# Kernel optimization log

Measured on AMD Instinct MI355X. Metric: run time of the kernel, lower is better.

## Reference

```python
import jax, jax.numpy as jnp
import numpy as np

B, H, N, Dh = 4, 16, 8192, 64
EPS = 1e-5          # masked-fill epsilon for D
CLAMP_EPS = 1e-10   # clamp_abs epsilon for gamma denominator
PROJ_EPS = 4e-3     # geoopt float32 projection epsilon


def _sumsq(x):
    return jnp.sum(x * x, axis=-1, keepdims=True)


def _pt0back(x, v, k):
    # geoopt parallel_transport0back: transport v from x back to origin
    # = v * lambda_x / lambda_0 = v / (1 + k ||x||^2)
    return v / jnp.maximum(1.0 + k * _sumsq(x), 1e-15)


def _lambda_x(x, k):
    # conformal factor 2 / (1 + k ||x||^2)
    return 2.0 / jnp.maximum(1.0 + k * _sumsq(x), 1e-15)


def _clamp_abs(x, eps):
    s = jnp.where(x >= 0, 1.0, -1.0)
    return s * jnp.maximum(jnp.abs(x), eps)


def _project(x, k):
    # clip points to the ball of radius (1-eps)/sqrt(|k|) when k < 0
    maxnorm = jnp.where(k < 0, (1.0 - PROJ_EPS) / jnp.sqrt(jnp.abs(k) + 1e-15), 1e15)
    norm = jnp.maximum(jnp.linalg.norm(x, axis=-1, keepdims=True), 1e-15)
    return jnp.where(norm > maxnorm, x / norm * maxnorm, x)


def _artan_k(u, k):
    sk = jnp.sqrt(jnp.abs(k) + 1e-15)
    su = sk * u
    hyp = jnp.arctanh(jnp.clip(su, -1.0 + 1e-7, 1.0 - 1e-7))
    return jnp.where(k < 0, hyp, jnp.arctan(su)) / sk


def _tan_k(u, k):
    sk = jnp.sqrt(jnp.abs(k) + 1e-15)
    su = sk * u
    return jnp.where(k < 0, jnp.tanh(su), jnp.tan(su)) / sk


def _mobius_scalar_mul(r, x, k):
    xnorm = jnp.maximum(jnp.linalg.norm(x, axis=-1, keepdims=True), 1e-15)
    return _tan_k(r * _artan_k(xnorm, k), k) * x / xnorm


def setup_inputs() -> dict:
    key = jax.random.key(0)
    kq, kk, kv = jax.random.split(key, 3)
    Q = 0.5 * jax.random.normal(kq, (B, H, N, Dh), dtype=jnp.float32)
    K = 0.5 * jax.random.normal(kk, (B, H, N, Dh), dtype=jnp.float32)
    # scale V so points lie well inside the Poincare ball: ||V||^2 ~ 0.16 < 1/|k|
    V = 0.05 * jax.random.normal(kv, (B, H, N, Dh), dtype=jnp.float32)
    mask = jnp.ones((N,), dtype=jnp.float32)
    curvatures = jnp.linspace(-2.0, -0.5, H, dtype=jnp.float32).reshape(H, 1, 1)
    return {"Q": Q, "K": K, "V": V, "mask": mask, "curvatures": curvatures}


def reference(Q, K, V, mask, curvatures):
    k = curvatures                      # [H,1,1], broadcasts over [B,H,N,1]
    m = mask[None, :, None]             # [1,N,1] -> broadcasts over [B,H,N,D]
    v1 = _pt0back(V, Q, k)              # transport Q from V back to origin
    v2 = _pt0back(V, K, k)
    gamma = _lambda_x(V, k)             # [B,H,N,1]
    denom = _clamp_abs(gamma - 1.0, CLAMP_EPS)
    x = gamma / denom * V * m           # [B,H,N,D]
    v1 = jax.nn.elu(v1) + 1.0           # positive feature map
    v2 = denom * (jax.nn.elu(v2) + 1.0) * m
    v2_sum = jnp.sum(v2, axis=-2)       # [B,H,D]
    Dn = jnp.einsum('bhnd,bhd->bhn', v1, v2_sum)
    D_inv = 1.0 / jnp.where(Dn == 0, EPS, Dn)
    context = jnp.einsum('bhnd,bhne->bhde', v2, x)          # [B,H,D,D]
    X = jnp.einsum('bhde,bhnd,bhn->bhne', context, v1, D_inv)
    X = _project(X, k)
    X = _mobius_scalar_mul(0.5, X, k)
    X = _project(X, k)
    return X
```

## Files before the change

kernel.cpp:

```cpp
#include <hip/hip_runtime.h>
#include <math.h>

#define NROWS   8192
#define DHH     64
#define BHCOUNT 64
#define HCOUNT  16
#define SPLITA  16
#define CHUNKA  (NROWS / SPLITA)
#define GA      32
#define LSTR    68
#define SPLITB  32
#define CHUNKB  (NROWS / SPLITB)
#define CTXSZ   4160
#define EPS_DN  1e-5f
#define PROJ_EPS 0.004f

__device__ __forceinline__ float elu1(float x) {
    return x > 0.0f ? x + 1.0f : expf(x);
}

__global__ __launch_bounds__(256) void phaseA(
        const float* __restrict__ Kp, const float* __restrict__ Vp,
        const float* __restrict__ maskp, const float* __restrict__ curvp,
        float* __restrict__ denomWs, float* __restrict__ partials) {
    __shared__ __align__(16) float v2s[GA * LSTR];
    __shared__ __align__(16) float xs[GA * LSTR];
    const int bx = blockIdx.x;
    const int bh = bx / SPLITA, sp = bx % SPLITA;
    const float k = curvp[bh % HCOUNT];
    const int t = threadIdx.x;
    const int rowBase = sp * CHUNKA;
    const float* Kb = Kp + (size_t)bh * NROWS * DHH;
    const float* Vb = Vp + (size_t)bh * NROWS * DHH;

    float acc[4][4] = {{0.f,0.f,0.f,0.f},{0.f,0.f,0.f,0.f},{0.f,0.f,0.f,0.f},{0.f,0.f,0.f,0.f}};
    float4 v2sum4 = make_float4(0.f, 0.f, 0.f, 0.f);
    const int rloc = t >> 4;
    const int c4   = t & 15;
    const int td   = t >> 4;
    const int te   = t & 15;

    for (int g = 0; g < CHUNKA / GA; ++g) {
        #pragma unroll
        for (int pass = 0; pass < 2; ++pass) {
            const int rl = pass * 16 + rloc;
            const int n = rowBase + g * GA + rl;
            const float4 v4 = *(const float4*)(Vb + (size_t)n * DHH + 4 * c4);
            const float4 k4 = *(const float4*)(Kb + (size_t)n * DHH + 4 * c4);
            float ss = v4.x*v4.x + v4.y*v4.y + v4.z*v4.z + v4.w*v4.w;
            ss += __shfl_xor(ss, 1);
            ss += __shfl_xor(ss, 2);
            ss += __shfl_xor(ss, 4);
            ss += __shfl_xor(ss, 8);
            const float dv    = fmaxf(1.0f + k * ss, 1e-15f);
            const float gamma = 2.0f / dv;
            const float gm1   = gamma - 1.0f;
            const float dnm   = (gm1 >= 0.0f ? 1.0f : -1.0f) * fmaxf(fabsf(gm1), 1e-10f);
            const float m     = maskp[n];
            const float idv   = 1.0f / dv;
            const float cv2   = dnm * m;
            const float cx    = (gamma / dnm) * m;
            float4 v2v, xv;
            v2v.x = cv2 * elu1(k4.x * idv);
            v2v.y = cv2 * elu1(k4.y * idv);
            v2v.z = cv2 * elu1(k4.z * idv);
            v2v.w = cv2 * elu1(k4.w * idv);
            xv.x = cx * v4.x; xv.y = cx * v4.y; xv.z = cx * v4.z; xv.w = cx * v4.w;
            *(float4*)&v2s[rl * LSTR + 4 * c4] = v2v;
            *(float4*)&xs [rl * LSTR + 4 * c4] = xv;
            v2sum4.x += v2v.x; v2sum4.y += v2v.y; v2sum4.z += v2v.z; v2sum4.w += v2v.w;
            if (c4 == 0) denomWs[(size_t)bh * NROWS + n] = dv;
        }
        __syncthreads();
        #pragma unroll 4
        for (int r = 0; r < GA; ++r) {
            const float4 a = *(const float4*)&v2s[r * LSTR + 4 * td];
            const float4 b = *(const float4*)&xs [r * LSTR + 4 * te];
            acc[0][0] += a.x*b.x; acc[0][1] += a.x*b.y; acc[0][2] += a.x*b.z; acc[0][3] += a.x*b.w;
            acc[1][0] += a.y*b.x; acc[1][1] += a.y*b.y; acc[1][2] += a.y*b.z; acc[1][3] += a.y*b.w;
            acc[2][0] += a.z*b.x; acc[2][1] += a.z*b.y; acc[2][2] += a.z*b.z; acc[2][3] += a.z*b.w;
            acc[3][0] += a.w*b.x; acc[3][1] += a.w*b.y; acc[3][2] += a.w*b.z; acc[3][3] += a.w*b.w;
        }
        __syncthreads();
    }

    float* pbase = partials + (size_t)(bh * SPLITA + sp) * CTXSZ;
    #pragma unroll
    for (int i = 0; i < 4; ++i) {
        float4 o = make_float4(acc[i][0], acc[i][1], acc[i][2], acc[i][3]);
        *(float4*)(pbase + (4 * td + i) * DHH + 4 * te) = o;
    }
    __syncthreads();
    *(float4*)&v2s[t * 4] = v2sum4;
    __syncthreads();
    if (t < DHH) {
        const int cc = t >> 2, j = t & 3;
        float s = 0.f;
        #pragma unroll
        for (int q = 0; q < 16; ++q) s += v2s[(q * 16 + cc) * 4 + j];
        pbase[4096 + t] = s;
    }
}

__global__ __launch_bounds__(256) void reduceCtx(
        const float* __restrict__ partials, float* __restrict__ ctxsum) {
    const int bh = blockIdx.x;
    const int t = threadIdx.x;
    for (int idx = t; idx < CTXSZ; idx += 256) {
        const float* p = partials + (size_t)bh * SPLITA * CTXSZ + idx;
        float s = 0.f;
        #pragma unroll
        for (int sp = 0; sp < SPLITA; ++sp) s += p[(size_t)sp * CTXSZ];
        ctxsum[(size_t)bh * CTXSZ + idx] = s;
    }
}

__global__ __launch_bounds__(256) void phaseB(
        const float* __restrict__ Qp, const float* __restrict__ curvp,
        const float* __restrict__ denomWs, const float* __restrict__ ctxsum,
        float* __restrict__ outp) {
    __shared__ __align__(16) float ctx[DHH * LSTR];
    __shared__ __align__(16) float v1s[64 * LSTR];
    __shared__ __align__(16) float v2sum[DHH];
    __shared__ float dinv[64];
    __shared__ float rowsq[64 * 17];
    __shared__ float factor[64];

    const int bx = blockIdx.x;
    const int bh = bx / SPLITB, sp = bx % SPLITB;
    const float k = curvp[bh % HCOUNT];
    const float sk = sqrtf(fabsf(k) + 1e-15f);
    const float maxnorm = (k < 0.0f) ? (1.0f - PROJ_EPS) / sk : 1e15f;
    const int t = threadIdx.x;

    const float* cb = ctxsum + (size_t)bh * CTXSZ;
    #pragma unroll
    for (int i = 0; i < 16; ++i) {
        const int idx = i * 256 + t;
        ctx[(idx >> 6) * LSTR + (idx & 63)] = cb[idx];
    }
    if (t < DHH) v2sum[t] = cb[4096 + t];
    __syncthreads();

    const float* Qb  = Qp  + (size_t)bh * NROWS * DHH;
    float*       Ob  = outp + (size_t)bh * NROWS * DHH;
    const float* dvb = denomWs + (size_t)bh * NROWS;
    const int rloc = t >> 4, c4 = t & 15;
    const int tr = t >> 4, tc = t & 15;

    for (int tile = 0; tile < CHUNKB / 64; ++tile) {
        const int n0 = sp * CHUNKB + tile * 64;
        #pragma unroll
        for (int pass = 0; pass < 4; ++pass) {
            const int rl = pass * 16 + rloc;
            const int n = n0 + rl;
            const float4 q4 = *(const float4*)(Qb + (size_t)n * DHH + 4 * c4);
            const float dv = dvb[n];
            const float idv = 1.0f / dv;
            float4 v14;
            v14.x = elu1(q4.x * idv);
            v14.y = elu1(q4.y * idv);
            v14.z = elu1(q4.z * idv);
            v14.w = elu1(q4.w * idv);
            *(float4*)&v1s[rl * LSTR + 4 * c4] = v14;
            const float4 vs = *(const float4*)&v2sum[4 * c4];
            float dn = v14.x * vs.x + v14.y * vs.y + v14.z * vs.z + v14.w * vs.w;
            dn += __shfl_xor(dn, 1);
            dn += __shfl_xor(dn, 2);
            dn += __shfl_xor(dn, 4);
            dn += __shfl_xor(dn, 8);
            if (c4 == 0) {
                const float Dd = (dn == 0.0f) ? EPS_DN : dn;
                dinv[rl] = 1.0f / Dd;
            }
        }
        __syncthreads();
        float acc[4][4] = {{0.f,0.f,0.f,0.f},{0.f,0.f,0.f,0.f},{0.f,0.f,0.f,0.f},{0.f,0.f,0.f,0.f}};
        #pragma unroll 8
        for (int d = 0; d < DHH; ++d) {
            const float4 cv = *(const float4*)&ctx[d * LSTR + 4 * tc];
            const float a0 = v1s[(4 * tr + 0) * LSTR + d];
            const float a1 = v1s[(4 * tr + 1) * LSTR + d];
            const float a2 = v1s[(4 * tr + 2) * LSTR + d];
            const float a3 = v1s[(4 * tr + 3) * LSTR + d];
            acc[0][0] += a0*cv.x; acc[0][1] += a0*cv.y; acc[0][2] += a0*cv.z; acc[0][3] += a0*cv.w;
            acc[1][0] += a1*cv.x; acc[1][1] += a1*cv.y; acc[1][2] += a1*cv.z; acc[1][3] += a1*cv.w;
            acc[2][0] += a2*cv.x; acc[2][1] += a2*cv.y; acc[2][2] += a2*cv.z; acc[2][3] += a2*cv.w;
            acc[3][0] += a3*cv.x; acc[3][1] += a3*cv.y; acc[3][2] += a3*cv.z; acc[3][3] += a3*cv.w;
        }
        #pragma unroll
        for (int i = 0; i < 4; ++i) {
            const float di = dinv[4 * tr + i];
            acc[i][0] *= di; acc[i][1] *= di; acc[i][2] *= di; acc[i][3] *= di;
            const float ps = acc[i][0]*acc[i][0] + acc[i][1]*acc[i][1]
                           + acc[i][2]*acc[i][2] + acc[i][3]*acc[i][3];
            rowsq[(4 * tr + i) * 17 + tc] = ps;
        }
        __syncthreads();
        if (t < 64) {
            float s = 0.f;
            #pragma unroll
            for (int q = 0; q < 16; ++q) s += rowsq[t * 17 + q];
            const float norm = fmaxf(sqrtf(s), 1e-15f);
            const float f1 = (norm > maxnorm) ? (maxnorm / norm) : 1.0f;
            const float n2 = norm * f1;
            const float xnorm = fmaxf(n2, 1e-15f);
            const float su = sk * xnorm;
            const float suc = fminf(su, 1.0f - 1e-7f);
            float tk;
            if (k < 0.0f) tk = tanhf(0.5f * atanhf(suc));
            else          tk = tanf(0.5f * atanf(su));
            tk = tk / sk;
            const float f2 = tk / xnorm;
            const float n3 = fmaxf(fabsf(tk), 1e-15f);
            const float f3 = (n3 > maxnorm) ? (maxnorm / n3) : 1.0f;
            factor[t] = f1 * f2 * f3;
        }
        __syncthreads();
        #pragma unroll
        for (int i = 0; i < 4; ++i) {
            const float f = factor[4 * tr + i];
            float4 o = make_float4(acc[i][0] * f, acc[i][1] * f, acc[i][2] * f, acc[i][3] * f);
            *(float4*)(Ob + (size_t)(n0 + 4 * tr + i) * DHH + 4 * tc) = o;
        }
        __syncthreads();
    }
}

extern "C" void kernel_launch(void* const* d_in, const int* in_sizes, int n_in,
                              void* d_out, int out_size, void* d_ws, size_t ws_size,
                              hipStream_t stream) {
    const float* Q    = (const float*)d_in[0];
    const float* K    = (const float*)d_in[1];
    const float* V    = (const float*)d_in[2];
    const float* mask = (const float*)d_in[3];
    const float* curv = (const float*)d_in[4];
    float* out = (float*)d_out;

    float* denomWs  = (float*)d_ws;
    float* partials = denomWs + (size_t)BHCOUNT * NROWS;
    float* ctxsum   = partials + (size_t)BHCOUNT * SPLITA * CTXSZ;

    phaseA<<<dim3(BHCOUNT * SPLITA), dim3(256), 0, stream>>>(K, V, mask, curv, denomWs, partials);
    reduceCtx<<<dim3(BHCOUNT), dim3(256), 0, stream>>>(partials, ctxsum);
    phaseB<<<dim3(BHCOUNT * SPLITB), dim3(256), 0, stream>>>(Q, curv, denomWs, ctxsum, out);
}
```

Baseline: 471.7 us.

## Replace partials reduction with atomics and streamline phaseB epilogue

PhaseA now accumulates context and v2 sums into a zeroed buffer with float atomicAdd instead of writing per-split partials, and a separate reduceCtx kernel. SPLITA doubles for more blocks. PhaseB keeps D_inv in registers, reduces row norms with warp shuffles instead of shared memory plus two barriers, uses float4 reads of v1 in the matmul, and replaces tanh(0.5*atanh) with an algebraic half-angle formula. Atomics make summation order nondeterministic and add contention, and a zero-fill kernel is added.

Result: slower. 534.2 us (+13.2%).

```diff
diff --git a/kernel.cpp b/kernel.cpp
--- a/kernel.cpp
+++ b/kernel.cpp
@@ -5,7 +5,7 @@
 #define DHH     64
 #define BHCOUNT 64
 #define HCOUNT  16
-#define SPLITA  16
+#define SPLITA  32
 #define CHUNKA  (NROWS / SPLITA)
 #define GA      32
 #define LSTR    68
@@ -19,10 +19,15 @@
     return x > 0.0f ? x + 1.0f : expf(x);
 }
 
+__global__ __launch_bounds__(256) void zeroCtx(float* __restrict__ p, int n) {
+    const int i = blockIdx.x * 256 + threadIdx.x;
+    if (i < n) p[i] = 0.0f;
+}
+
 __global__ __launch_bounds__(256) void phaseA(
         const float* __restrict__ Kp, const float* __restrict__ Vp,
         const float* __restrict__ maskp, const float* __restrict__ curvp,
-        float* __restrict__ denomWs, float* __restrict__ partials) {
+        float* __restrict__ denomWs, float* __restrict__ ctxsum) {
     __shared__ __align__(16) float v2s[GA * LSTR];
     __shared__ __align__(16) float xs[GA * LSTR];
     const int bx = blockIdx.x;
@@ -84,11 +89,13 @@
         __syncthreads();
     }
 
-    float* pbase = partials + (size_t)(bh * SPLITA + sp) * CTXSZ;
+    float* cbase = ctxsum + (size_t)bh * CTXSZ;
     #pragma unroll
     for (int i = 0; i < 4; ++i) {
-        float4 o = make_float4(acc[i][0], acc[i][1], acc[i][2], acc[i][3]);
-        *(float4*)(pbase + (4 * td + i) * DHH + 4 * te) = o;
+        atomicAdd(&cbase[(4 * td + i) * DHH + 4 * te + 0], acc[i][0]);
+        atomicAdd(&cbase[(4 * td + i) * DHH + 4 * te + 1], acc[i][1]);
+        atomicAdd(&cbase[(4 * td + i) * DHH + 4 * te + 2], acc[i][2]);
+        atomicAdd(&cbase[(4 * td + i) * DHH + 4 * te + 3], acc[i][3]);
     }
     __syncthreads();
     *(float4*)&v2s[t * 4] = v2sum4;
@@ -98,20 +105,7 @@
         float s = 0.f;
         #pragma unroll
         for (int q = 0; q < 16; ++q) s += v2s[(q * 16 + cc) * 4 + j];
-        pbase[4096 + t] = s;
-    }
-}
-
-__global__ __launch_bounds__(256) void reduceCtx(
-        const float* __restrict__ partials, float* __restrict__ ctxsum) {
-    const int bh = blockIdx.x;
-    const int t = threadIdx.x;
-    for (int idx = t; idx < CTXSZ; idx += 256) {
-        const float* p = partials + (size_t)bh * SPLITA * CTXSZ + idx;
-        float s = 0.f;
-        #pragma unroll
-        for (int sp = 0; sp < SPLITA; ++sp) s += p[(size_t)sp * CTXSZ];
-        ctxsum[(size_t)bh * CTXSZ + idx] = s;
+        atomicAdd(&cbase[4096 + t], s);
     }
 }
 
@@ -122,9 +116,6 @@
     __shared__ __align__(16) float ctx[DHH * LSTR];
     __shared__ __align__(16) float v1s[64 * LSTR];
     __shared__ __align__(16) float v2sum[DHH];
-    __shared__ float dinv[64];
-    __shared__ float rowsq[64 * 17];
-    __shared__ float factor[64];
 
     const int bx = blockIdx.x;
     const int bh = bx / SPLITB, sp = bx % SPLITB;
@@ -132,6 +123,7 @@
     const float sk = sqrtf(fabsf(k) + 1e-15f);
     const float maxnorm = (k < 0.0f) ? (1.0f - PROJ_EPS) / sk : 1e15f;
     const int t = threadIdx.x;
+    const int tr = t >> 4, tc = t & 15;
 
     const float* cb = ctxsum + (size_t)bh * CTXSZ;
     #pragma unroll
@@ -145,82 +137,73 @@
     const float* Qb  = Qp  + (size_t)bh * NROWS * DHH;
     float*       Ob  = outp + (size_t)bh * NROWS * DHH;
     const float* dvb = denomWs + (size_t)bh * NROWS;
-    const int rloc = t >> 4, c4 = t & 15;
-    const int tr = t >> 4, tc = t & 15;
 
     for (int tile = 0; tile < CHUNKB / 64; ++tile) {
         const int n0 = sp * CHUNKB + tile * 64;
+        float di[4];
         #pragma unroll
         for (int pass = 0; pass < 4; ++pass) {
-            const int rl = pass * 16 + rloc;
+            const int rl = 4 * tr + pass;
             const int n = n0 + rl;
-            const float4 q4 = *(const float4*)(Qb + (size_t)n * DHH + 4 * c4);
-            const float dv = dvb[n];
-            const float idv = 1.0f / dv;
+            const float4 q4 = *(const float4*)(Qb + (size_t)n * DHH + 4 * tc);
+            const float idv = 1.0f / dvb[n];
             float4 v14;
             v14.x = elu1(q4.x * idv);
             v14.y = elu1(q4.y * idv);
             v14.z = elu1(q4.z * idv);
             v14.w = elu1(q4.w * idv);
-            *(float4*)&v1s[rl * LSTR + 4 * c4] = v14;
-            const float4 vs = *(const float4*)&v2sum[4 * c4];
+            *(float4*)&v1s[rl * LSTR + 4 * tc] = v14;
+            const float4 vs = *(const float4*)&v2sum[4 * tc];
             float dn = v14.x * vs.x + v14.y * vs.y + v14.z * vs.z + v14.w * vs.w;
             dn += __shfl_xor(dn, 1);
             dn += __shfl_xor(dn, 2);
             dn += __shfl_xor(dn, 4);
             dn += __shfl_xor(dn, 8);
-            if (c4 == 0) {
-                const float Dd = (dn == 0.0f) ? EPS_DN : dn;
-                dinv[rl] = 1.0f / Dd;
+            const float Dd = (dn == 0.0f) ? EPS_DN : dn;
+            di[pass] = 1.0f / Dd;
+        }
+        __syncthreads();
+        float acc[4][4] = {{0.f,0.f,0.f,0.f},{0.f,0.f,0.f,0.f},{0.f,0.f,0.f,0.f},{0.f,0.f,0.f,0.f}};
+        #pragma unroll 4
+        for (int db = 0; db < 16; ++db) {
+            const float4 c0 = *(const float4*)&ctx[(4 * db + 0) * LSTR + 4 * tc];
+            const float4 c1 = *(const float4*)&ctx[(4 * db + 1) * LSTR + 4 * tc];
+            const float4 c2 = *(const float4*)&ctx[(4 * db + 2) * LSTR + 4 * tc];
+            const float4 c3 = *(const float4*)&ctx[(4 * db + 3) * LSTR + 4 * tc];
+            #pragma unroll
+            for (int i = 0; i < 4; ++i) {
+                const float4 a = *(const float4*)&v1s[(4 * tr + i) * LSTR + 4 * db];
+                acc[i][0] += a.x*c0.x + a.y*c1.x + a.z*c2.x + a.w*c3.x;
+                acc[i][1] += a.x*c0.y + a.y*c1.y + a.z*c2.y + a.w*c3.y;
+                acc[i][2] += a.x*c0.z + a.y*c1.z + a.z*c2.z + a.w*c3.z;
+                acc[i][3] += a.x*c0.w + a.y*c1.w + a.z*c2.w + a.w*c3.w;
             }
         }
-        __syncthreads();
-        float acc[4][4] = {{0.f,0.f,0.f,0.f},{0.f,0.f,0.f,0.f},{0.f,0.f,0.f,0.f},{0.f,0.f,0.f,0.f}};
-        #pragma unroll 8
-        for (int d = 0; d < DHH; ++d) {
-            const float4 cv = *(const float4*)&ctx[d * LSTR + 4 * tc];
-            const float a0 = v1s[(4 * tr + 0) * LSTR + d];
-            const float a1 = v1s[(4 * tr + 1) * LSTR + d];
-            const float a2 = v1s[(4 * tr + 2) * LSTR + d];
-            const float a3 = v1s[(4 * tr + 3) * LSTR + d];
-            acc[0][0] += a0*cv.x; acc[0][1] += a0*cv.y; acc[0][2] += a0*cv.z; acc[0][3] += a0*cv.w;
-            acc[1][0] += a1*cv.x; acc[1][1] += a1*cv.y; acc[1][2] += a1*cv.z; acc[1][3] += a1*cv.w;
-            acc[2][0] += a2*cv.x; acc[2][1] += a2*cv.y; acc[2][2] += a2*cv.z; acc[2][3] += a2*cv.w;
-            acc[3][0] += a3*cv.x; acc[3][1] += a3*cv.y; acc[3][2] += a3*cv.z; acc[3][3] += a3*cv.w;
-        }
         #pragma unroll
         for (int i = 0; i < 4; ++i) {
-            const float di = dinv[4 * tr + i];
-            acc[i][0] *= di; acc[i][1] *= di; acc[i][2] *= di; acc[i][3] *= di;
-            const float ps = acc[i][0]*acc[i][0] + acc[i][1]*acc[i][1]
-                           + acc[i][2]*acc[i][2] + acc[i][3]*acc[i][3];
-            rowsq[(4 * tr + i) * 17 + tc] = ps;
-        }
-        __syncthreads();
-        if (t < 64) {
-            float s = 0.f;
-            #pragma unroll
-            for (int q = 0; q < 16; ++q) s += rowsq[t * 17 + q];
-            const float norm = fmaxf(sqrtf(s), 1e-15f);
+            float ps = acc[i][0]*acc[i][0] + acc[i][1]*acc[i][1]
+                     + acc[i][2]*acc[i][2] + acc[i][3]*acc[i][3];
+            ps += __shfl_xor(ps, 1);
+            ps += __shfl_xor(ps, 2);
+            ps += __shfl_xor(ps, 4);
+            ps += __shfl_xor(ps, 8);
+            const float norm = fmaxf(di[i] * sqrtf(ps), 1e-15f);
             const float f1 = (norm > maxnorm) ? (maxnorm / norm) : 1.0f;
-            const float n2 = norm * f1;
-            const float xnorm = fmaxf(n2, 1e-15f);
+            const float xnorm = fmaxf(norm * f1, 1e-15f);
             const float su = sk * xnorm;
-            const float suc = fminf(su, 1.0f - 1e-7f);
             float tk;
-            if (k < 0.0f) tk = tanhf(0.5f * atanhf(suc));
-            else          tk = tanf(0.5f * atanf(su));
+            if (k < 0.0f) {
+                const float suc = fminf(su, 1.0f - 1e-7f);
+                tk = suc / (1.0f + sqrtf(fmaxf(1.0f - suc * suc, 0.0f)));
+            } else {
+                tk = su / (1.0f + sqrtf(1.0f + su * su));
+            }
             tk = tk / sk;
             const float f2 = tk / xnorm;
             const float n3 = fmaxf(fabsf(tk), 1e-15f);
             const float f3 = (n3 > maxnorm) ? (maxnorm / n3) : 1.0f;
-            factor[t] = f1 * f2 * f3;
-        }
-        __syncthreads();
-        #pragma unroll
-        for (int i = 0; i < 4; ++i) {
-            const float f = factor[4 * tr + i];
-            float4 o = make_float4(acc[i][0] * f, acc[i][1] * f, acc[i][2] * f, acc[i][3] * f);
+            const float fs = di[i] * f1 * f2 * f3;
+            float4 o = make_float4(acc[i][0] * fs, acc[i][1] * fs, acc[i][2] * fs, acc[i][3] * fs);
             *(float4*)(Ob + (size_t)(n0 + 4 * tr + i) * DHH + 4 * tc) = o;
         }
         __syncthreads();
@@ -237,11 +220,11 @@
     const float* curv = (const float*)d_in[4];
     float* out = (float*)d_out;
 
-    float* denomWs  = (float*)d_ws;
-    float* partials = denomWs + (size_t)BHCOUNT * NROWS;
-    float* ctxsum   = partials + (size_t)BHCOUNT * SPLITA * CTXSZ;
-
-    phaseA<<<dim3(BHCOUNT * SPLITA), dim3(256), 0, stream>>>(K, V, mask, curv, denomWs, partials);
-    reduceCtx<<<dim3(BHCOUNT), dim3(256), 0, stream>>>(partials, ctxsum);
+    float* denomWs = (float*)d_ws;
+    float* ctxsum  = denomWs + (size_t)BHCOUNT * NROWS;
+
+    const int ctxTotal = BHCOUNT * CTXSZ;
+    zeroCtx<<<dim3((ctxTotal + 255) / 256), dim3(256), 0, stream>>>(ctxsum, ctxTotal);
+    phaseA<<<dim3(BHCOUNT * SPLITA), dim3(256), 0, stream>>>(K, V, mask, curv, denomWs, ctxsum);
     phaseB<<<dim3(BHCOUNT * SPLITB), dim3(256), 0, stream>>>(Q, curv, denomWs, ctxsum, out);
 }
```
